# Optimization experiments

Hardware: AMD Instinct MI355X
Metric: run time of the kernel (lower is better)

Reference implementation:

```python
import jax, jax.numpy as jnp
from jax import lax
import numpy as np

B, Hn, Wn = 128, 39, 39          # batch graphs, rows, cols (nodes per graph = Wn)
N = B * Wn                        # total nodes = 4992
HEADS, HID, OUT = 8, 64, 64
E_PER = 1563                      # edges per graph -> 200064 total
EPS = 1e-5                        # BatchNorm eps (eval mode, running mean=0 var=1)


def setup_inputs():
    key = jax.random.key(0)
    ks = jax.random.split(key, 32)
    rn = lambda k, shp, s: jax.random.normal(k, shp, jnp.float32) * s
    inp = {}
    inp['edge_index_batch'] = jax.random.randint(ks[0], (2, B, E_PER), 0, N)
    inp['ve_matrix_batch'] = rn(ks[1], (B, Hn, Wn), 1.0)
    inp['ac_matrix_batch'] = rn(ks[2], (B, Hn, Wn), 1.0)
    inp['man_matrix_batch'] = rn(ks[3], (B, Hn, Wn), 1.0)
    inp['mask_view_batch'] = jax.random.uniform(ks[4], (B, Wn, 1), jnp.float32)
    inp['graph_matrix'] = jnp.zeros((B, 2 * Hn, Wn), jnp.float32)
    # conv stack params
    inp['conv1_w'] = rn(ks[5], (8, 3, 1, 1), 1.0 / np.sqrt(3.0))
    inp['conv1_b'] = jnp.zeros((8,), jnp.float32)
    inp['bn1_g'] = jnp.ones((8,), jnp.float32)
    inp['bn1_b'] = jnp.zeros((8,), jnp.float32)
    inp['conv2_w'] = rn(ks[6], (16, 8, 3, 3), 1.0 / np.sqrt(8.0 * 9.0))
    inp['conv2_b'] = jnp.zeros((16,), jnp.float32)
    inp['bn2_g'] = jnp.ones((16,), jnp.float32)
    inp['bn2_b'] = jnp.zeros((16,), jnp.float32)
    # GRU(16 -> 1) params (torch layout: W_ih (3*h, in), W_hh (3*h, h))
    inp['gru_wih'] = rn(ks[7], (3, 16), 0.25)
    inp['gru_whh'] = rn(ks[8], (3, 1), 0.5)
    inp['gru_bih'] = jnp.zeros((3,), jnp.float32)
    inp['gru_bhh'] = jnp.zeros((3,), jnp.float32)
    # GATv2 layer 1: 78 -> (8 heads x 64)
    inp['g1_wl'] = rn(ks[9], (HEADS * HID, 78), 1.0 / np.sqrt(78.0))
    inp['g1_bl'] = jnp.zeros((HEADS * HID,), jnp.float32)
    inp['g1_wr'] = rn(ks[10], (HEADS * HID, 78), 1.0 / np.sqrt(78.0))
    inp['g1_br'] = jnp.zeros((HEADS * HID,), jnp.float32)
    inp['g1_att'] = rn(ks[11], (HEADS, HID), 1.0 / np.sqrt(HID))
    inp['g1_bias'] = jnp.zeros((HEADS * HID,), jnp.float32)
    # GATv2 layer 2: 512 -> (1 head x 64)
    inp['g2_wl'] = rn(ks[12], (OUT, HEADS * HID), 1.0 / np.sqrt(HEADS * HID))
    inp['g2_bl'] = jnp.zeros((OUT,), jnp.float32)
    inp['g2_wr'] = rn(ks[13], (OUT, HEADS * HID), 1.0 / np.sqrt(HEADS * HID))
    inp['g2_br'] = jnp.zeros((OUT,), jnp.float32)
    inp['g2_att'] = rn(ks[14], (1, OUT), 1.0 / np.sqrt(OUT))
    inp['g2_bias'] = jnp.zeros((OUT,), jnp.float32)
    return inp


def _conv2d(x, w, b, pad):
    y = lax.conv_general_dilated(x, w, (1, 1), [(pad, pad), (pad, pad)],
                                 dimension_numbers=('NCHW', 'OIHW', 'NCHW'))
    return y + b[None, :, None, None]


def _bn_eval(x, g, b):
    # eval-mode BatchNorm2d with fresh running stats (mean=0, var=1)
    return x * (g / jnp.sqrt(1.0 + EPS))[None, :, None, None] + b[None, :, None, None]


def _gatv2(x, src, dst, Wl, bl, Wr, br, att, bo, heads, ch):
    # PyG GATv2Conv: alpha = softmax_dst(att . leaky_relu(xl[src] + xr[dst]))
    xl = (x @ Wl.T + bl).reshape(-1, heads, ch)
    xr = (x @ Wr.T + br).reshape(-1, heads, ch)
    e = jax.nn.leaky_relu(xl[src] + xr[dst], 0.2)            # (E, heads, ch)
    logit = jnp.einsum('ehc,hc->eh', e, att)                 # (E, heads)
    m = jax.ops.segment_max(logit, dst, num_segments=N)
    ex = jnp.exp(logit - m[dst])
    den = jax.ops.segment_sum(ex, dst, num_segments=N)
    alpha = ex / den[dst]
    out = jax.ops.segment_sum(xl[src] * alpha[:, :, None], dst, num_segments=N)
    return out.reshape(-1, heads * ch) + bo


def reference(edge_index_batch, ve_matrix_batch, ac_matrix_batch, man_matrix_batch,
              mask_view_batch, graph_matrix, conv1_w, conv1_b, bn1_g, bn1_b,
              conv2_w, conv2_b, bn2_g, bn2_b, gru_wih, gru_whh, gru_bih, gru_bhh,
              g1_wl, g1_bl, g1_wr, g1_br, g1_att, g1_bias,
              g2_wl, g2_bl, g2_wr, g2_br, g2_att, g2_bias):
    man = jnp.where(jnp.isnan(man_matrix_batch), 0.0, man_matrix_batch)
    ac = jnp.where(jnp.isnan(ac_matrix_batch), 0.0, ac_matrix_batch)
    ve = jnp.where(jnp.isnan(ve_matrix_batch), 0.0, ve_matrix_batch)

    cm = jnp.stack([man, ac, ve], axis=1)                    # (B,3,H,W)
    x = jax.nn.relu(_bn_eval(_conv2d(cm, conv1_w, conv1_b, 0), bn1_g, bn1_b))
    x = _bn_eval(_conv2d(x, conv2_w, conv2_b, 1), bn2_g, bn2_b)  # (B,16,H,W); dropout=eval

    # GRU(16->1) over rows, batched across (graph, column) instead of a python loop
    xs = jnp.transpose(x, (2, 0, 3, 1)).reshape(Hn, B * Wn, 16)  # (T=H, B*W, 16)

    def step(h, xt):
        gi = xt @ gru_wih.T + gru_bih                        # (BW, 3)
        gh = h @ gru_whh.T + gru_bhh                         # (BW, 3)
        r = jax.nn.sigmoid(gi[:, 0:1] + gh[:, 0:1])
        z = jax.nn.sigmoid(gi[:, 1:2] + gh[:, 1:2])
        n = jnp.tanh(gi[:, 2:3] + r * gh[:, 2:3])
        hn = (1.0 - z) * n + z * h
        return hn, hn

    h0 = jnp.zeros((B * Wn, 1), x.dtype)
    _, outs = lax.scan(step, h0, xs)                         # (H, B*W, 1)
    conv_enc1 = jnp.transpose(outs.reshape(Hn, B, Wn), (1, 0, 2))  # (B,H,W)

    mask = mask_view_batch.reshape(B, -1)[:, None, :]        # (B,1,W)
    conv_enc2 = conv_enc1 * mask
    man2 = man * mask
    g = jnp.concatenate([man2, conv_enc2], axis=1)           # (B,78,W)  (graph_matrix input is overwritten)
    xn = jnp.transpose(g, (0, 2, 1)).reshape(N, 2 * Hn)      # (N,78)

    edges = edge_index_batch.reshape(2, -1)
    loop = jnp.arange(N)                                     # PyG add_self_loops=True
    src = jnp.concatenate([edges[0], loop])
    dst = jnp.concatenate([edges[1], loop])

    h1 = jax.nn.elu(_gatv2(xn, src, dst, g1_wl, g1_bl, g1_wr, g1_br, g1_att, g1_bias, HEADS, HID))
    h2 = _gatv2(h1, src, dst, g2_wl, g2_bl, g2_wr, g2_br, g2_att, g2_bias, 1, OUT)
    return h2.reshape(B, Wn, OUT)                            # (128, 39, 64)
```

## Files before the change

### kernel.cpp

```cpp
#include <hip/hip_runtime.h>
#include <hip/hip_bf16.h>
#include <math.h>

#define HN 39
#define WN 39
#define NBATCH 128
#define NPIX (HN * WN)
#define NNODE (NBATCH * WN)
#define E_RAW 200064
#define E_TOT (E_RAW + NNODE)
#define F1 512
#define F2 64
#define CROWS 6
#define GIPL (NBATCH * NPIX)

static __device__ __forceinline__ float nan0(float x) { return (x == x) ? x : 0.f; }
static __device__ __forceinline__ float sigmoid_f(float x) { return 1.f / (1.f + __expf(-x)); }
static __device__ __forceinline__ float tanh_f(float x) {
    float e = __expf(2.f * x);
    return 1.f - 2.f / (e + 1.f);
}

#define BN_RSQ 0.99999500003749969f

__global__ __launch_bounds__(256) void conv_kernel(
    const float* __restrict__ ve, const float* __restrict__ ac, const float* __restrict__ man,
    const float* __restrict__ c1w, const float* __restrict__ c1b,
    const float* __restrict__ bn1g, const float* __restrict__ bn1b,
    const float* __restrict__ c2w, const float* __restrict__ c2b,
    const float* __restrict__ bn2g, const float* __restrict__ bn2b,
    const float* __restrict__ wih, const float* __restrict__ bih,
    const float* __restrict__ maskv,
    float* __restrict__ gi_out,
    float* __restrict__ xn)
{
    __shared__ float y1[8][(CROWS + 2) * WN + 8];
    const int b = blockIdx.x;
    const int r0 = blockIdx.y * CROWS;
    const int tid = threadIdx.x;

    for (int p = tid; p < (CROWS + 2) * WN; p += 256) {
        const int row = p / WN;
        const int hh = r0 - 1 + row;
        if (hh < 0 || hh >= HN) continue;
        const int w = p - row * WN;
        const int gidx = b * NPIX + hh * WN + w;
        const float m = nan0(man[gidx]);
        const float a = nan0(ac[gidx]);
        const float v = nan0(ve[gidx]);
        if (hh >= r0 && hh < r0 + CROWS)
            xn[(size_t)(b * WN + w) * 78 + hh] = m * maskv[b * WN + w];
#pragma unroll
        for (int c = 0; c < 8; ++c) {
            float val = c1w[c * 3 + 0] * m + c1w[c * 3 + 1] * a + c1w[c * 3 + 2] * v + c1b[c];
            val = val * (bn1g[c] * BN_RSQ) + bn1b[c];
            y1[c][p] = fmaxf(val, 0.f);
        }
    }
    __syncthreads();

    for (int p = tid; p < CROWS * WN; p += 256) {
        const int h = r0 + p / WN;
        if (h >= HN) continue;
        const int w = p - (p / WN) * WN;
        float acc[16];
#pragma unroll
        for (int o = 0; o < 16; ++o) acc[o] = 0.f;
        for (int c = 0; c < 8; ++c) {
#pragma unroll
            for (int dy = 0; dy < 3; ++dy) {
                const int hh = h + dy - 1;
                if (hh < 0 || hh >= HN) continue;
                const int lrow = hh - r0 + 1;
#pragma unroll
                for (int dx = 0; dx < 3; ++dx) {
                    const int ww = w + dx - 1;
                    if (ww < 0 || ww >= WN) continue;
                    const float yv = y1[c][lrow * WN + ww];
#pragma unroll
                    for (int o = 0; o < 16; ++o)
                        acc[o] = fmaf(c2w[((o * 8 + c) * 3 + dy) * 3 + dx], yv, acc[o]);
                }
            }
        }
        float gi0 = bih[0], gi1 = bih[1], gi2 = bih[2];
#pragma unroll
        for (int o = 0; o < 16; ++o) {
            const float x2 = (acc[o] + c2b[o]) * (bn2g[o] * BN_RSQ) + bn2b[o];
            gi0 = fmaf(wih[0 * 16 + o], x2, gi0);
            gi1 = fmaf(wih[1 * 16 + o], x2, gi1);
            gi2 = fmaf(wih[2 * 16 + o], x2, gi2);
        }
        const int idx = b * NPIX + h * WN + w;
        gi_out[idx] = gi0;
        gi_out[GIPL + idx] = gi1;
        gi_out[2 * GIPL + idx] = gi2;
    }
}

__global__ __launch_bounds__(64) void gru_kernel(
    const float* __restrict__ gi, const float* __restrict__ whh, const float* __restrict__ bhh,
    const float* __restrict__ maskv, float* __restrict__ xn)
{
    const int idx = blockIdx.x * 64 + threadIdx.x;
    if (idx >= NNODE) return;
    const int b = idx / WN, w = idx - (idx / WN) * WN;
    const float mk = maskv[idx];
    float* __restrict__ xrow = xn + (size_t)idx * 78 + HN;

    const float* __restrict__ g0 = gi + b * NPIX + w;
    const float* __restrict__ g1 = g0 + GIPL;
    const float* __restrict__ g2 = g0 + 2 * GIPL;

    const float wh0 = whh[0], wh1 = whh[1], wh2 = whh[2];
    const float bh0 = bhh[0], bh1 = bhh[1], bh2 = bhh[2];
    float h = 0.f;
#pragma unroll 1
    for (int t = 0; t < HN; t += 3) {
        const float ga0 = g0[t * WN],       ga1 = g1[t * WN],       ga2 = g2[t * WN];
        const float gb0 = g0[(t + 1) * WN], gb1 = g1[(t + 1) * WN], gb2 = g2[(t + 1) * WN];
        const float gc0 = g0[(t + 2) * WN], gc1 = g1[(t + 2) * WN], gc2 = g2[(t + 2) * WN];

        float r = sigmoid_f(ga0 + h * wh0 + bh0);
        float z = sigmoid_f(ga1 + h * wh1 + bh1);
        float n = tanh_f(ga2 + r * (h * wh2 + bh2));
        h = (1.f - z) * n + z * h;
        xrow[t] = h * mk;

        r = sigmoid_f(gb0 + h * wh0 + bh0);
        z = sigmoid_f(gb1 + h * wh1 + bh1);
        n = tanh_f(gb2 + r * (h * wh2 + bh2));
        h = (1.f - z) * n + z * h;
        xrow[t + 1] = h * mk;

        r = sigmoid_f(gc0 + h * wh0 + bh0);
        z = sigmoid_f(gc1 + h * wh1 + bh1);
        n = tanh_f(gc2 + r * (h * wh2 + bh2));
        h = (1.f - z) * n + z * h;
        xrow[t + 2] = h * mk;
    }
}

__global__ __launch_bounds__(256) void edge_hist(const int* __restrict__ ei, int* __restrict__ counts)
{
    const int e = blockIdx.x * 256 + threadIdx.x;
    if (e >= E_TOT) return;
    const int d = (e < E_RAW) ? ei[E_RAW + e] : (e - E_RAW);
    atomicAdd(&counts[d], 1);
}

__global__ __launch_bounds__(256) void scan_kernel(const int* __restrict__ counts,
                                                   int* __restrict__ offsets, int* __restrict__ cursor)
{
    __shared__ int sums[256];
    const int tid = threadIdx.x;
    const int start = tid * 20;
    const int end = min(start + 20, NNODE);
    int s = 0;
    for (int i = start; i < end; ++i) s += counts[i];
    sums[tid] = s;
    __syncthreads();
    for (int off = 1; off < 256; off <<= 1) {
        int v = (tid >= off) ? sums[tid - off] : 0;
        __syncthreads();
        sums[tid] += v;
        __syncthreads();
    }
    int run = (tid == 0) ? 0 : sums[tid - 1];
    for (int i = start; i < end; ++i) {
        offsets[i] = run;
        cursor[i] = run;
        run += counts[i];
    }
    if (tid == 255) offsets[NNODE] = run;
}

__global__ __launch_bounds__(256) void edge_scatter(const int* __restrict__ ei,
                                                    int* __restrict__ cursor,
                                                    int* __restrict__ srcs)
{
    const int e = blockIdx.x * 256 + threadIdx.x;
    if (e >= E_TOT) return;
    int s, d;
    if (e < E_RAW) { s = ei[e]; d = ei[E_RAW + e]; }
    else           { s = d = e - E_RAW; }
    const int pos = atomicAdd(&cursor[d], 1);
    srcs[pos] = s;
}

template <int K, int NZ>
__global__ __launch_bounds__(256, 4) void gemm_kernel(
    const float* __restrict__ X,
    const float* __restrict__ Wl, const float* __restrict__ bl,
    const float* __restrict__ Wr, const float* __restrict__ br,
    float* __restrict__ Yl, float* __restrict__ Yr, int J)
{
    const int nyb = J >> 6;
    const int sel = (blockIdx.y >= nyb) ? 1 : 0;
    const int j0 = (blockIdx.y - sel * nyb) * 64;
    const float* __restrict__ W = sel ? Wr : Wl;
    const float* __restrict__ bias = sel ? br : bl;
    float* __restrict__ Y;
    if (NZ == 1) Y = sel ? Yr : Yl;
    else         Y = Yl + ((size_t)blockIdx.z * 2 + sel) * ((size_t)NNODE * J);

    __shared__ __align__(16) float Xs[32][68];
    __shared__ __align__(16) float Ws[32][68];

    const int kchunk = K / NZ;
    const int kbeg = blockIdx.z * kchunk;
    const int kend = (blockIdx.z == NZ - 1) ? K : kbeg + kchunk;

    const int m0 = blockIdx.x * 64;
    const int tid = threadIdx.x;
    const int ti = tid / 16, tj = tid & 15;
    const int lrow = tid >> 2;
    const int ks = (tid & 3) * 8;

    float acc[4][4];
#pragma unroll
    for (int i = 0; i < 4; ++i)
#pragma unroll
        for (int j = 0; j < 4; ++j) acc[i][j] = 0.f;

    for (int k0 = kbeg; k0 < kend; k0 += 32) {
        const float* xp = X + (size_t)(m0 + lrow) * K + k0 + ks;
        const float* wp = W + (size_t)(j0 + lrow) * K + k0 + ks;
#pragma unroll
        for (int q = 0; q < 8; ++q) {
            const int k = k0 + ks + q;
            Xs[ks + q][lrow] = (k < K) ? xp[q] : 0.f;
            Ws[ks + q][lrow] = (k < K) ? wp[q] : 0.f;
        }
        __syncthreads();
#pragma unroll 8
        for (int kk = 0; kk < 32; ++kk) {
            const float4 xv = *(const float4*)&Xs[kk][ti * 4];
            const float4 wv = *(const float4*)&Ws[kk][tj * 4];
            acc[0][0] = fmaf(xv.x, wv.x, acc[0][0]);
            acc[0][1] = fmaf(xv.x, wv.y, acc[0][1]);
            acc[0][2] = fmaf(xv.x, wv.z, acc[0][2]);
            acc[0][3] = fmaf(xv.x, wv.w, acc[0][3]);
            acc[1][0] = fmaf(xv.y, wv.x, acc[1][0]);
            acc[1][1] = fmaf(xv.y, wv.y, acc[1][1]);
            acc[1][2] = fmaf(xv.y, wv.z, acc[1][2]);
            acc[1][3] = fmaf(xv.y, wv.w, acc[1][3]);
            acc[2][0] = fmaf(xv.z, wv.x, acc[2][0]);
            acc[2][1] = fmaf(xv.z, wv.y, acc[2][1]);
            acc[2][2] = fmaf(xv.z, wv.z, acc[2][2]);
            acc[2][3] = fmaf(xv.z, wv.w, acc[2][3]);
            acc[3][0] = fmaf(xv.w, wv.x, acc[3][0]);
            acc[3][1] = fmaf(xv.w, wv.y, acc[3][1]);
            acc[3][2] = fmaf(xv.w, wv.z, acc[3][2]);
            acc[3][3] = fmaf(xv.w, wv.w, acc[3][3]);
        }
        __syncthreads();
    }
#pragma unroll
    for (int i = 0; i < 4; ++i) {
        const int m = m0 + ti * 4 + i;
#pragma unroll
        for (int j = 0; j < 4; ++j) {
            const int jj = j0 + tj * 4 + j;
            if (NZ == 1) Y[(size_t)m * J + jj] = acc[i][j] + bias[jj];
            else         Y[(size_t)m * J + jj] = acc[i][j];
        }
    }
}

template <int NZ>
__global__ __launch_bounds__(256) void reduce_kernel(
    const float* __restrict__ P, const float* __restrict__ bl, const float* __restrict__ br,
    float* __restrict__ Yl, float* __restrict__ Yr)
{
    const int idx = blockIdx.x * 256 + threadIdx.x;
    const int per_side = NNODE * 64 / 4;
    if (idx >= 2 * per_side) return;
    const int side = idx >= per_side;
    const int r = idx - side * per_side;
    const int j4 = (r & 15);

    const float4* __restrict__ P4 = (const float4*)P;
    float4 acc = P4[(size_t)side * per_side + r];
#pragma unroll
    for (int z = 1; z < NZ; ++z) {
        const float4 v = P4[((size_t)z * 2 + side) * per_side + r];
        acc.x += v.x; acc.y += v.y; acc.z += v.z; acc.w += v.w;
    }
    const float4 bv = *(const float4*)((side ? br : bl) + j4 * 4);
    acc.x += bv.x; acc.y += bv.y; acc.z += bv.z; acc.w += bv.w;
    ((float4*)(side ? Yr : Yl))[r] = acc;
}

template <int FDIM>
static __device__ __forceinline__ void gat_nomax(
    const float* __restrict__ xl, const int* __restrict__ srcs,
    int base, int deg, int hoff, int lane, float4 xrv, float4 av,
    float4& accOut, float& lOut)
{
    const int e4 = lane >> 4;
    const int c4 = lane & 15;
    float l = 0.f;
    float4 acc = make_float4(0.f, 0.f, 0.f, 0.f);

    for (int c0 = 0; c0 < deg; c0 += 8) {
        const int eA = c0 + e4;
        const int eB = c0 + 4 + e4;
        const int sA = srcs[base + min(eA, deg - 1)];
        const int sB = srcs[base + min(eB, deg - 1)];
        const float4 xaA = *(const float4*)(xl + (size_t)sA * FDIM + hoff + c4 * 4);
        const float4 xaB = *(const float4*)(xl + (size_t)sB * FDIM + hoff + c4 * 4);

        float a0 = xaA.x + xrv.x; a0 = fmaxf(a0, 0.2f * a0);
        float a1 = xaA.y + xrv.y; a1 = fmaxf(a1, 0.2f * a1);
        float a2 = xaA.z + xrv.z; a2 = fmaxf(a2, 0.2f * a2);
        float a3 = xaA.w + xrv.w; a3 = fmaxf(a3, 0.2f * a3);
        float pA = av.x * a0 + av.y * a1 + av.z * a2 + av.w * a3;
        float b0 = xaB.x + xrv.x; b0 = fmaxf(b0, 0.2f * b0);
        float b1 = xaB.y + xrv.y; b1 = fmaxf(b1, 0.2f * b1);
        float b2 = xaB.z + xrv.z; b2 = fmaxf(b2, 0.2f * b2);
        float b3 = xaB.w + xrv.w; b3 = fmaxf(b3, 0.2f * b3);
        float pB = av.x * b0 + av.y * b1 + av.z * b2 + av.w * b3;

        pA += __shfl_xor(pA, 1, 64);
        pA += __shfl_xor(pA, 2, 64);
        pA += __shfl_xor(pA, 4, 64);
        pA += __shfl_xor(pA, 8, 64);
        pB += __shfl_xor(pB, 1, 64);
        pB += __shfl_xor(pB, 2, 64);
        pB += __shfl_xor(pB, 4, 64);
        pB += __shfl_xor(pB, 8, 64);

        const float wA = (eA < deg) ? __expf(pA) : 0.f;
        const float wB = (eB < deg) ? __expf(pB) : 0.f;
        l += wA + wB;
        acc.x = fmaf(wA, xaA.x, fmaf(wB, xaB.x, acc.x));
        acc.y = fmaf(wA, xaA.y, fmaf(wB, xaB.y, acc.y));
        acc.z = fmaf(wA, xaA.z, fmaf(wB, xaB.z, acc.z));
        acc.w = fmaf(wA, xaA.w, fmaf(wB, xaB.w, acc.w));
    }

    l += __shfl_xor(l, 16, 64);
    l += __shfl_xor(l, 32, 64);
    acc.x += __shfl_xor(acc.x, 16, 64);
    acc.y += __shfl_xor(acc.y, 16, 64);
    acc.z += __shfl_xor(acc.z, 16, 64);
    acc.w += __shfl_xor(acc.w, 16, 64);
    acc.x += __shfl_xor(acc.x, 32, 64);
    acc.y += __shfl_xor(acc.y, 32, 64);
    acc.z += __shfl_xor(acc.z, 32, 64);
    acc.w += __shfl_xor(acc.w, 32, 64);
    accOut = acc;
    lOut = l;
}

__global__ __launch_bounds__(512) void gat1_fused_kernel(
    const float* __restrict__ xl, const float* __restrict__ xr,
    const float* __restrict__ att, const float* __restrict__ bias,
    const int* __restrict__ offsets, const int* __restrict__ srcs,
    float* __restrict__ h1)
{
    const int n = blockIdx.x;
    const int h = threadIdx.x >> 6;
    const int lane = threadIdx.x & 63;
    const int base = offsets[n];
    const int deg = offsets[n + 1] - base;
    const int c4 = lane & 15;

    const float4 xrv = *(const float4*)(xr + (size_t)n * F1 + h * 64 + c4 * 4);
    const float4 av  = *(const float4*)(att + h * 64 + c4 * 4);

    float4 acc; float l;
    gat_nomax<F1>(xl, srcs, base, deg, h * 64, lane, xrv, av, acc, l);

    if ((lane >> 4) == 0) {
        const float inv = 1.f / l;
        const float4 bv = *(const float4*)(bias + h * 64 + c4 * 4);
        float4 o;
        o.x = acc.x * inv + bv.x; o.x = (o.x > 0.f) ? o.x : expm1f(o.x);
        o.y = acc.y * inv + bv.y; o.y = (o.y > 0.f) ? o.y : expm1f(o.y);
        o.z = acc.z * inv + bv.z; o.z = (o.z > 0.f) ? o.z : expm1f(o.z);
        o.w = acc.w * inv + bv.w; o.w = (o.w > 0.f) ? o.w : expm1f(o.w);
        *(float4*)(h1 + (size_t)n * F1 + h * 64 + c4 * 4) = o;
    }
}

__global__ __launch_bounds__(256) void gat2_fused_kernel(
    const float* __restrict__ xl, const float* __restrict__ xr,
    const float* __restrict__ att, const float* __restrict__ bias,
    const int* __restrict__ offsets, const int* __restrict__ srcs,
    float* __restrict__ out)
{
    const int wv = threadIdx.x >> 6;
    const int lane = threadIdx.x & 63;
    const int n = blockIdx.x * 4 + wv;
    const int base = offsets[n];
    const int deg = offsets[n + 1] - base;
    const int c4 = lane & 15;

    const float4 xrv = *(const float4*)(xr + (size_t)n * F2 + c4 * 4);
    const float4 av  = *(const float4*)(att + c4 * 4);

    float4 acc; float l;
    gat_nomax<F2>(xl, srcs, base, deg, 0, lane, xrv, av, acc, l);

    if ((lane >> 4) == 0) {
        const float inv = 1.f / l;
        const float4 bv = *(const float4*)(bias + c4 * 4);
        float4 o;
        o.x = acc.x * inv + bv.x;
        o.y = acc.y * inv + bv.y;
        o.z = acc.z * inv + bv.z;
        o.w = acc.w * inv + bv.w;
        *(float4*)(out + (size_t)n * F2 + c4 * 4) = o;
    }
}

extern "C" void kernel_launch(void* const* d_in, const int* in_sizes, int n_in,
                              void* d_out, int out_size, void* d_ws, size_t ws_size,
                              hipStream_t stream)
{
    const int*   ei    = (const int*)d_in[0];
    const float* ve    = (const float*)d_in[1];
    const float* ac    = (const float*)d_in[2];
    const float* man   = (const float*)d_in[3];
    const float* maskv = (const float*)d_in[4];
    const float* c1w   = (const float*)d_in[6];
    const float* c1b   = (const float*)d_in[7];
    const float* bn1g  = (const float*)d_in[8];
    const float* bn1b  = (const float*)d_in[9];
    const float* c2w   = (const float*)d_in[10];
    const float* c2b   = (const float*)d_in[11];
    const float* bn2g  = (const float*)d_in[12];
    const float* bn2b  = (const float*)d_in[13];
    const float* wih   = (const float*)d_in[14];
    const float* whh   = (const float*)d_in[15];
    const float* bih   = (const float*)d_in[16];
    const float* bhh   = (const float*)d_in[17];
    const float* g1wl  = (const float*)d_in[18];
    const float* g1bl  = (const float*)d_in[19];
    const float* g1wr  = (const float*)d_in[20];
    const float* g1br  = (const float*)d_in[21];
    const float* g1att = (const float*)d_in[22];
    const float* g1bias= (const float*)d_in[23];
    const float* g2wl  = (const float*)d_in[24];
    const float* g2bl  = (const float*)d_in[25];
    const float* g2wr  = (const float*)d_in[26];
    const float* g2br  = (const float*)d_in[27];
    const float* g2att = (const float*)d_in[28];
    const float* g2bias= (const float*)d_in[29];
    float* outp = (float*)d_out;

    float* ws     = (float*)d_ws;
    float* gi     = ws;
    float* xn     = gi     + 584064;
    float* xl1    = xn     + 389376;
    float* xr1    = xl1    + 2555904;
    float* h1     = xr1    + 2555904;
    float* xl2    = h1     + 2555904;
    float* xr2    = xl2    + 319488;
    int* counts  = (int*)(xr2 + 319488);
    int* offsets = counts + NNODE;
    int* cursor  = offsets + NNODE + 1;
    int* srcs    = cursor + NNODE;

    float* part = xl1;

    hipMemsetAsync(counts, 0, NNODE * sizeof(int), stream);

    conv_kernel<<<dim3(NBATCH, (HN + CROWS - 1) / CROWS), 256, 0, stream>>>(
        ve, ac, man, c1w, c1b, bn1g, bn1b, c2w, c2b, bn2g, bn2b, wih, bih,
        maskv, gi, xn);
    gru_kernel<<<(NNODE + 63) / 64, 64, 0, stream>>>(gi, whh, bhh, maskv, xn);

    edge_hist<<<(E_TOT + 255) / 256, 256, 0, stream>>>(ei, counts);
    scan_kernel<<<1, 256, 0, stream>>>(counts, offsets, cursor);
    edge_scatter<<<(E_TOT + 255) / 256, 256, 0, stream>>>(ei, cursor, srcs);

    gemm_kernel<78, 1><<<dim3(NNODE / 64, 2 * (F1 / 64)), 256, 0, stream>>>(
        xn, g1wl, g1bl, g1wr, g1br, xl1, xr1, F1);

    gat1_fused_kernel<<<NNODE, 512, 0, stream>>>(xl1, xr1, g1att, g1bias, offsets, srcs, h1);

    gemm_kernel<512, 8><<<dim3(NNODE / 64, 2 * (F2 / 64), 8), 256, 0, stream>>>(
        h1, g2wl, g2bl, g2wr, g2br, part, nullptr, F2);
    reduce_kernel<8><<<(2 * NNODE * 64 / 4 + 255) / 256, 256, 0, stream>>>(
        part, g2bl, g2br, xl2, xr2);

    gat2_fused_kernel<<<NNODE / 4, 256, 0, stream>>>(xl2, xr2, g2att, g2bias, offsets, srcs, outp);
}
```

Measured before the change: 306.2 us.

## Merge independent small kernels into shared launches to cut launch overhead

The counts memset moves into the conv kernel. The GRU recurrence and the edge histogram now run as block ranges of one launch, and the edge scatter shares a launch with the layer-1 GEMM, which is inlined as a specialised copy of the generic GEMM. The goal is fewer kernel launches and serialisation gaps, and letting the latency-bound GRU overlap with the atomic-heavy histogram. In exchange, the GRU blocks go from 64 to 256 threads, so fewer blocks carry the recurrence. The GEMM tile loop may also differ from the templated version.

```diff
diff --git a/kernel.cpp b/kernel.cpp
--- a/kernel.cpp
+++ b/kernel.cpp
@@ -13,6 +13,8 @@
 #define F2 64
 #define CROWS 6
 #define GIPL (NBATCH * NPIX)
+#define HIST_BLKS 802
+#define GRU_BLKS 20
 
 static __device__ __forceinline__ float nan0(float x) { return (x == x) ? x : 0.f; }
 static __device__ __forceinline__ float sigmoid_f(float x) { return 1.f / (1.f + __expf(-x)); }
@@ -32,12 +34,15 @@
     const float* __restrict__ wih, const float* __restrict__ bih,
     const float* __restrict__ maskv,
     float* __restrict__ gi_out,
-    float* __restrict__ xn)
+    float* __restrict__ xn,
+    int* __restrict__ counts)
 {
     __shared__ float y1[8][(CROWS + 2) * WN + 8];
     const int b = blockIdx.x;
     const int r0 = blockIdx.y * CROWS;
     const int tid = threadIdx.x;
+
+    if (blockIdx.y == 0 && tid < WN) counts[b * WN + tid] = 0;
 
     for (int p = tid; p < (CROWS + 2) * WN; p += 256) {
         const int row = p / WN;
@@ -98,55 +103,56 @@
     }
 }
 
-__global__ __launch_bounds__(64) void gru_kernel(
+__global__ __launch_bounds__(256) void gru_hist_kernel(
     const float* __restrict__ gi, const float* __restrict__ whh, const float* __restrict__ bhh,
-    const float* __restrict__ maskv, float* __restrict__ xn)
-{
-    const int idx = blockIdx.x * 64 + threadIdx.x;
-    if (idx >= NNODE) return;
-    const int b = idx / WN, w = idx - (idx / WN) * WN;
-    const float mk = maskv[idx];
-    float* __restrict__ xrow = xn + (size_t)idx * 78 + HN;
-
-    const float* __restrict__ g0 = gi + b * NPIX + w;
-    const float* __restrict__ g1 = g0 + GIPL;
-    const float* __restrict__ g2 = g0 + 2 * GIPL;
-
-    const float wh0 = whh[0], wh1 = whh[1], wh2 = whh[2];
-    const float bh0 = bhh[0], bh1 = bhh[1], bh2 = bhh[2];
-    float h = 0.f;
+    const float* __restrict__ maskv, float* __restrict__ xn,
+    const int* __restrict__ ei, int* __restrict__ counts)
+{
+    const int blk = blockIdx.x;
+    if (blk < GRU_BLKS) {
+        const int idx = blk * 256 + threadIdx.x;
+        if (idx >= NNODE) return;
+        const int b = idx / WN, w = idx - (idx / WN) * WN;
+        const float mk = maskv[idx];
+        float* __restrict__ xrow = xn + (size_t)idx * 78 + HN;
+
+        const float* __restrict__ g0 = gi + b * NPIX + w;
+        const float* __restrict__ g1 = g0 + GIPL;
+        const float* __restrict__ g2 = g0 + 2 * GIPL;
+
+        const float wh0 = whh[0], wh1 = whh[1], wh2 = whh[2];
+        const float bh0 = bhh[0], bh1 = bhh[1], bh2 = bhh[2];
+        float h = 0.f;
 #pragma unroll 1
-    for (int t = 0; t < HN; t += 3) {
-        const float ga0 = g0[t * WN],       ga1 = g1[t * WN],       ga2 = g2[t * WN];
-        const float gb0 = g0[(t + 1) * WN], gb1 = g1[(t + 1) * WN], gb2 = g2[(t + 1) * WN];
-        const float gc0 = g0[(t + 2) * WN], gc1 = g1[(t + 2) * WN], gc2 = g2[(t + 2) * WN];
-
-        float r = sigmoid_f(ga0 + h * wh0 + bh0);
-        float z = sigmoid_f(ga1 + h * wh1 + bh1);
-        float n = tanh_f(ga2 + r * (h * wh2 + bh2));
-        h = (1.f - z) * n + z * h;
-        xrow[t] = h * mk;
-
-        r = sigmoid_f(gb0 + h * wh0 + bh0);
-        z = sigmoid_f(gb1 + h * wh1 + bh1);
-        n = tanh_f(gb2 + r * (h * wh2 + bh2));
-        h = (1.f - z) * n + z * h;
-        xrow[t + 1] = h * mk;
-
-        r = sigmoid_f(gc0 + h * wh0 + bh0);
-        z = sigmoid_f(gc1 + h * wh1 + bh1);
-        n = tanh_f(gc2 + r * (h * wh2 + bh2));
-        h = (1.f - z) * n + z * h;
-        xrow[t + 2] = h * mk;
-    }
-}
-
-__global__ __launch_bounds__(256) void edge_hist(const int* __restrict__ ei, int* __restrict__ counts)
-{
-    const int e = blockIdx.x * 256 + threadIdx.x;
-    if (e >= E_TOT) return;
-    const int d = (e < E_RAW) ? ei[E_RAW + e] : (e - E_RAW);
-    atomicAdd(&counts[d], 1);
+        for (int t = 0; t < HN; t += 3) {
+            const float ga0 = g0[t * WN],       ga1 = g1[t * WN],       ga2 = g2[t * WN];
+            const float gb0 = g0[(t + 1) * WN], gb1 = g1[(t + 1) * WN], gb2 = g2[(t + 1) * WN];
+            const float gc0 = g0[(t + 2) * WN], gc1 = g1[(t + 2) * WN], gc2 = g2[(t + 2) * WN];
+
+            float r = sigmoid_f(ga0 + h * wh0 + bh0);
+            float z = sigmoid_f(ga1 + h * wh1 + bh1);
+            float n = tanh_f(ga2 + r * (h * wh2 + bh2));
+            h = (1.f - z) * n + z * h;
+            xrow[t] = h * mk;
+
+            r = sigmoid_f(gb0 + h * wh0 + bh0);
+            z = sigmoid_f(gb1 + h * wh1 + bh1);
+            n = tanh_f(gb2 + r * (h * wh2 + bh2));
+            h = (1.f - z) * n + z * h;
+            xrow[t + 1] = h * mk;
+
+            r = sigmoid_f(gc0 + h * wh0 + bh0);
+            z = sigmoid_f(gc1 + h * wh1 + bh1);
+            n = tanh_f(gc2 + r * (h * wh2 + bh2));
+            h = (1.f - z) * n + z * h;
+            xrow[t + 2] = h * mk;
+        }
+    } else {
+        const int e = (blk - GRU_BLKS) * 256 + threadIdx.x;
+        if (e >= E_TOT) return;
+        const int d = (e < E_RAW) ? ei[E_RAW + e] : (e - E_RAW);
+        atomicAdd(&counts[d], 1);
+    }
 }
 
 __global__ __launch_bounds__(256) void scan_kernel(const int* __restrict__ counts,
@@ -175,17 +181,90 @@
     if (tid == 255) offsets[NNODE] = run;
 }
 
-__global__ __launch_bounds__(256) void edge_scatter(const int* __restrict__ ei,
-                                                    int* __restrict__ cursor,
-                                                    int* __restrict__ srcs)
-{
-    const int e = blockIdx.x * 256 + threadIdx.x;
-    if (e >= E_TOT) return;
-    int s, d;
-    if (e < E_RAW) { s = ei[e]; d = ei[E_RAW + e]; }
-    else           { s = d = e - E_RAW; }
-    const int pos = atomicAdd(&cursor[d], 1);
-    srcs[pos] = s;
+__global__ __launch_bounds__(256) void scatter_gemm78_kernel(
+    const int* __restrict__ ei, int* __restrict__ cursor, int* __restrict__ srcs,
+    const float* __restrict__ X,
+    const float* __restrict__ Wl, const float* __restrict__ bl,
+    const float* __restrict__ Wr, const float* __restrict__ br,
+    float* __restrict__ Yl, float* __restrict__ Yr)
+{
+    if (blockIdx.x < HIST_BLKS) {
+        const int e = blockIdx.x * 256 + threadIdx.x;
+        if (e >= E_TOT) return;
+        int s, d;
+        if (e < E_RAW) { s = ei[e]; d = ei[E_RAW + e]; }
+        else           { s = d = e - E_RAW; }
+        const int pos = atomicAdd(&cursor[d], 1);
+        srcs[pos] = s;
+        return;
+    }
+
+    const int bx = blockIdx.x - HIST_BLKS;
+    const int m0 = (bx % 78) * 64;
+    const int yt = bx / 78;
+    const int sel = (yt >= 8) ? 1 : 0;
+    const int j0 = (yt - sel * 8) * 64;
+    const float* __restrict__ W = sel ? Wr : Wl;
+    const float* __restrict__ bias = sel ? br : bl;
+    float* __restrict__ Y = sel ? Yr : Yl;
+    const int K = 78, J = F1;
+
+    __shared__ __align__(16) float Xs[32][68];
+    __shared__ __align__(16) float Ws[32][68];
+
+    const int tid = threadIdx.x;
+    const int ti = tid / 16, tj = tid & 15;
+    const int lrow = tid >> 2;
+    const int ks = (tid & 3) * 8;
+
+    float acc[4][4];
+#pragma unroll
+    for (int i = 0; i < 4; ++i)
+#pragma unroll
+        for (int j = 0; j < 4; ++j) acc[i][j] = 0.f;
+
+    for (int k0 = 0; k0 < K; k0 += 32) {
+        const float* xp = X + (size_t)(m0 + lrow) * K + k0 + ks;
+        const float* wp = W + (size_t)(j0 + lrow) * K + k0 + ks;
+#pragma unroll
+        for (int q = 0; q < 8; ++q) {
+            const int k = k0 + ks + q;
+            Xs[ks + q][lrow] = (k < K) ? xp[q] : 0.f;
+            Ws[ks + q][lrow] = (k < K) ? wp[q] : 0.f;
+        }
+        __syncthreads();
+#pragma unroll 8
+        for (int kk = 0; kk < 32; ++kk) {
+            const float4 xv = *(const float4*)&Xs[kk][ti * 4];
+            const float4 wv = *(const float4*)&Ws[kk][tj * 4];
+            acc[0][0] = fmaf(xv.x, wv.x, acc[0][0]);
+            acc[0][1] = fmaf(xv.x, wv.y, acc[0][1]);
+            acc[0][2] = fmaf(xv.x, wv.z, acc[0][2]);
+            acc[0][3] = fmaf(xv.x, wv.w, acc[0][3]);
+            acc[1][0] = fmaf(xv.y, wv.x, acc[1][0]);
+            acc[1][1] = fmaf(xv.y, wv.y, acc[1][1]);
+            acc[1][2] = fmaf(xv.y, wv.z, acc[1][2]);
+            acc[1][3] = fmaf(xv.y, wv.w, acc[1][3]);
+            acc[2][0] = fmaf(xv.z, wv.x, acc[2][0]);
+            acc[2][1] = fmaf(xv.z, wv.y, acc[2][1]);
+            acc[2][2] = fmaf(xv.z, wv.z, acc[2][2]);
+            acc[2][3] = fmaf(xv.z, wv.w, acc[2][3]);
+            acc[3][0] = fmaf(xv.w, wv.x, acc[3][0]);
+            acc[3][1] = fmaf(xv.w, wv.y, acc[3][1]);
+            acc[3][2] = fmaf(xv.w, wv.z, acc[3][2]);
+            acc[3][3] = fmaf(xv.w, wv.w, acc[3][3]);
+        }
+        __syncthreads();
+    }
+#pragma unroll
+    for (int i = 0; i < 4; ++i) {
+        const int m = m0 + ti * 4 + i;
+#pragma unroll
+        for (int j = 0; j < 4; ++j) {
+            const int jj = j0 + tj * 4 + j;
+            Y[(size_t)m * J + jj] = acc[i][j] + bias[jj];
+        }
+    }
 }
 
 template <int K, int NZ>
@@ -466,19 +545,17 @@
 
     float* part = xl1;
 
-    hipMemsetAsync(counts, 0, NNODE * sizeof(int), stream);
-
     conv_kernel<<<dim3(NBATCH, (HN + CROWS - 1) / CROWS), 256, 0, stream>>>(
         ve, ac, man, c1w, c1b, bn1g, bn1b, c2w, c2b, bn2g, bn2b, wih, bih,
-        maskv, gi, xn);
-    gru_kernel<<<(NNODE + 63) / 64, 64, 0, stream>>>(gi, whh, bhh, maskv, xn);
-
-    edge_hist<<<(E_TOT + 255) / 256, 256, 0, stream>>>(ei, counts);
+        maskv, gi, xn, counts);
+
+    gru_hist_kernel<<<GRU_BLKS + HIST_BLKS, 256, 0, stream>>>(
+        gi, whh, bhh, maskv, xn, ei, counts);
+
     scan_kernel<<<1, 256, 0, stream>>>(counts, offsets, cursor);
-    edge_scatter<<<(E_TOT + 255) / 256, 256, 0, stream>>>(ei, cursor, srcs);
-
-    gemm_kernel<78, 1><<<dim3(NNODE / 64, 2 * (F1 / 64)), 256, 0, stream>>>(
-        xn, g1wl, g1bl, g1wr, g1br, xl1, xr1, F1);
+
+    scatter_gemm78_kernel<<<HIST_BLKS + 78 * 16, 256, 0, stream>>>(
+        ei, cursor, srcs, xn, g1wl, g1bl, g1wr, g1br, xl1, xr1);
 
     gat1_fused_kernel<<<NNODE, 512, 0, stream>>>(xl1, xr1, g1att, g1bias, offsets, srcs, h1);
 
```

After: 280.3 us. 1.09x faster.
